# Kernel tuning notes

Measured on AMD Instinct MI355X. Metric: run time of the kernel, lower is better.

## Reference

```python
import jax, jax.numpy as jnp
import numpy as np
import math

N_WIRES = 8

def _cnot(state, ctrl, tgt):
    # state: (N, 2,2,...,2) with wire w on axis 1+w
    c_ax = 1 + ctrl
    t_ax = 1 + tgt
    s0 = jnp.take(state, 0, axis=c_ax)
    s1 = jnp.take(state, 1, axis=c_ax)
    t2 = t_ax - 1 if t_ax > c_ax else t_ax
    s1 = jnp.flip(s1, axis=t2)
    return jnp.stack([s0, s1], axis=c_ax)

def _qlayer(x, phi):
    # x: (N, 8) encoder RX angles; phi: (8,) trainable RX angles.
    # encoder RX(x_i) followed by RX(phi_i) on the same wire == RX(x_i + phi_i)
    N = x.shape[0]
    half = 0.5 * (x + phi)
    c = jnp.cos(half).astype(jnp.complex64)
    s = jnp.sin(half).astype(jnp.complex64)
    amp = jnp.stack([c, (-1j) * s], axis=-1)  # (N, 8, 2) per-wire RX|0>
    # product state via successive outer products -> (N, 2,...,2)
    state = amp[:, 0]
    for w in range(1, N_WIRES):
        q = amp[:, w].reshape((N,) + (1,) * w + (2,))
        state = state[..., None] * q
    # CNOT ring
    for w in range(N_WIRES - 1):
        state = _cnot(state, w, w + 1)
    state = _cnot(state, N_WIRES - 1, 0)
    probs = state.real ** 2 + state.imag ** 2  # (N, 2,...,2)
    exps = []
    for w in range(N_WIRES):
        axes = tuple(a for a in range(1, N_WIRES + 1) if a != 1 + w)
        pw = jnp.sum(probs, axis=axes)  # (N, 2)
        exps.append(pw[:, 0] - pw[:, 1])  # <Z_w>
    return jnp.stack(exps, axis=-1)  # (N, 8)


def setup_inputs() -> dict:
    key = jax.random.key(0)
    k1, k2, k3 = jax.random.split(key, 3)
    B, S, E = 4, 1024, 128
    x = jax.random.normal(k1, (B, S, E), jnp.float32)
    phi = jax.random.normal(k2, (N_WIRES,), jnp.float32)
    W = jax.random.normal(k3, (E, E), jnp.float32) / math.sqrt(E)
    b = jnp.zeros((E,), jnp.float32)
    return {"x": x, "phi": phi, "W": W, "b": b}


def reference(x, phi, W, b):
    B, S, E = x.shape
    H = 16
    d = N_WIRES  # head dim == n_wires == 8
    xh = x.reshape(B, S, H, d).reshape(-1, d)
    proj = _qlayer(xh, phi).reshape(B, S, H, d)
    # q, k, v are identical (same layer, same input, deterministic) -> compute once
    q = jnp.transpose(proj, (0, 2, 1, 3))  # (B, H, S, d)
    scores = jnp.einsum('bhqd,bhkd->bhqk', q, q) / math.sqrt(d)
    attn = jax.nn.softmax(scores, axis=-1)  # dropout: eval mode (identity)
    out = jnp.einsum('bhqk,bhkd->bhqd', attn, q)
    out = jnp.transpose(out, (0, 2, 1, 3)).reshape(B, S, E)
    return out @ W.T + b
```

## Files before the change

kernel.cpp:

```cpp
#include <hip/hip_runtime.h>

#define NB 4
#define NS 1024
#define NE 128
#define NH 16
#define ND 8

typedef __attribute__((ext_vector_type(4))) _Float16 half4v;
typedef __attribute__((ext_vector_type(8))) _Float16 half8v;
typedef __attribute__((ext_vector_type(2))) _Float16 half2v;
typedef __attribute__((ext_vector_type(4))) float float4v;

#if __has_builtin(__builtin_amdgcn_exp2f)
#define EXP2F(x) __builtin_amdgcn_exp2f(x)
#else
#define EXP2F(x) __expf(0.69314718055994531f * (x))
#endif

#define SQRT_ALPHA 0.71423656f

#define MFMA32(A, B, C) __builtin_amdgcn_mfma_f32_16x16x32_f16((A), (B), (C), 0, 0, 0)

static __device__ __forceinline__ half8v cat8(half4v lo, half4v hi) {
    return __builtin_shufflevector(lo, hi, 0, 1, 2, 3, 4, 5, 6, 7);
}
static __device__ __forceinline__ half4v cat4(half2v lo, half2v hi) {
    return __builtin_shufflevector(lo, hi, 0, 1, 2, 3);
}

__global__ __launch_bounds__(512, 4)
void qattn_kernel(const float* __restrict__ x, const float* __restrict__ phi,
                  float* __restrict__ aout)
{
    __shared__ __align__(16) _Float16 Klds[NS][8];
    __shared__ __align__(16) _Float16 Vt[9][1036];
    __shared__ __align__(16) float4 scratch[2][2][4][64];

    const int t    = threadIdx.x;
    const int blk  = blockIdx.x;
    const int qt   = blk & 7;
    const int bh   = blk >> 3;
    const int b    = bh >> 4;
    const int h    = bh & 15;
    const int lane = t & 63;
    const int w    = t >> 6;
    const int qg   = w & 1;
    const int kh   = w >> 1;

    const float ph0 = phi[0], ph1 = phi[1], ph2 = phi[2], ph3 = phi[3];
    const float ph4 = phi[4], ph5 = phi[5], ph6 = phi[6], ph7 = phi[7];

    {
        const float* xb = x + ((size_t)b * NS) * NE + h * ND;
        const int k0 = t, k1 = t + 512;
        float4 xa0 = *(const float4*)(xb + (size_t)k0 * NE);
        float4 xc0 = *(const float4*)(xb + (size_t)k0 * NE + 4);
        float4 xa1 = *(const float4*)(xb + (size_t)k1 * NE);
        float4 xc1 = *(const float4*)(xb + (size_t)k1 * NE + 4);
#pragma unroll
        for (int half = 0; half < 2; ++half) {
            const int k = half ? k1 : k0;
            const float4 xa = half ? xa1 : xa0;
            const float4 xc = half ? xc1 : xc0;
            float g0 = __cosf(xa.x + ph0), g1 = __cosf(xa.y + ph1);
            float g2 = __cosf(xa.z + ph2), g3 = __cosf(xa.w + ph3);
            float g4 = __cosf(xc.x + ph4), g5 = __cosf(xc.y + ph5);
            float g6 = __cosf(xc.z + ph6), g7 = __cosf(xc.w + ph7);
            float s7 = g7, s6 = s7 * g6, s5 = s6 * g5, s4 = s5 * g4, s3 = s4 * g3, s2 = s3 * g2;
            float v0 = s2 * g1;
            float v1 = g0 * g1, v2 = v1 * g2, v3 = v2 * g3;
            float v4 = v3 * g4, v5 = v4 * g5, v6 = v5 * g6, v7 = v6 * g7;
            half8v row;
            row[0] = (_Float16)(SQRT_ALPHA * v0); row[1] = (_Float16)(SQRT_ALPHA * v1);
            row[2] = (_Float16)(SQRT_ALPHA * v2); row[3] = (_Float16)(SQRT_ALPHA * v3);
            row[4] = (_Float16)(SQRT_ALPHA * v4); row[5] = (_Float16)(SQRT_ALPHA * v5);
            row[6] = (_Float16)(SQRT_ALPHA * v6); row[7] = (_Float16)(SQRT_ALPHA * v7);
            *(half8v*)&Klds[k][0] = row;
            Vt[0][k] = (_Float16)v0; Vt[1][k] = (_Float16)v1;
            Vt[2][k] = (_Float16)v2; Vt[3][k] = (_Float16)v3;
            Vt[4][k] = (_Float16)v4; Vt[5][k] = (_Float16)v5;
            Vt[6][k] = (_Float16)v6; Vt[7][k] = (_Float16)v7;
            Vt[8][k] = (_Float16)1.0f;
        }
    }
    __syncthreads();

    const int e = lane & 15;
    const int g = lane >> 4;
    const half4v zero4 = (half4v)(_Float16)0.0f;

    half4v qf0 = zero4, qf1 = zero4, qf2 = zero4, qf3 = zero4;
    if (lane < 32) {
        const int qbase = qt * 128 + qg * 64 + e;
        qf0 = *(const half4v*)&Klds[qbase][g * 4];
        qf1 = *(const half4v*)&Klds[qbase + 16][g * 4];
        qf2 = *(const half4v*)&Klds[qbase + 32][g * 4];
        qf3 = *(const half4v*)&Klds[qbase + 48][g * 4];
    }
    const half8v qf80 = cat8(qf0, zero4);
    const half8v qf81 = cat8(qf1, zero4);
    const half8v qf82 = cat8(qf2, zero4);
    const half8v qf83 = cat8(qf3, zero4);

    const _Float16* kp = &Klds[kh * 256 + e][(g & 1) * 4];
    const int ecl = (e > 8) ? 8 : e;
    const _Float16* vp = &Vt[ecl][kh * 256 + g * 4];

    float4v acc0 = (float4v)0.0f;
    float4v acc1 = (float4v)0.0f;
    float4v acc2 = (float4v)0.0f;
    float4v acc3 = (float4v)0.0f;
    const float4v zero = (float4v)0.0f;

#pragma unroll 1
    for (int p = 0; p < 8; ++p) {
        const _Float16* kpp = kp + p * 256;
        const _Float16* vpp = vp + p * 32;

        half4v kf0 = *(const half4v*)(kpp);
        half4v kf1 = *(const half4v*)(kpp + 128);
        half4v vf0 = *(const half4v*)(vpp);
        half4v vf1 = *(const half4v*)(vpp + 16);
        half8v kf80 = cat8(kf0, zero4);
        half8v kf81 = cat8(kf1, zero4);
        half8v vf8  = cat8(vf0, vf1);

        __builtin_amdgcn_s_setprio(1);
        float4v s00 = MFMA32(kf80, qf80, zero);
        float4v s01 = MFMA32(kf80, qf81, zero);
        float4v s02 = MFMA32(kf80, qf82, zero);
        float4v s03 = MFMA32(kf80, qf83, zero);
        float p000 = EXP2F(s00[0]), p001 = EXP2F(s00[1]), p002 = EXP2F(s00[2]), p003 = EXP2F(s00[3]);
        float p010 = EXP2F(s01[0]), p011 = EXP2F(s01[1]), p012 = EXP2F(s01[2]), p013 = EXP2F(s01[3]);
        float p020 = EXP2F(s02[0]), p021 = EXP2F(s02[1]), p022 = EXP2F(s02[2]), p023 = EXP2F(s02[3]);
        float p030 = EXP2F(s03[0]), p031 = EXP2F(s03[1]), p032 = EXP2F(s03[2]), p033 = EXP2F(s03[3]);
        half4v paA0 = cat4(__builtin_bit_cast(half2v, __builtin_amdgcn_cvt_pkrtz(p000, p001)),
                           __builtin_bit_cast(half2v, __builtin_amdgcn_cvt_pkrtz(p002, p003)));
        half4v paA1 = cat4(__builtin_bit_cast(half2v, __builtin_amdgcn_cvt_pkrtz(p010, p011)),
                           __builtin_bit_cast(half2v, __builtin_amdgcn_cvt_pkrtz(p012, p013)));
        half4v paA2 = cat4(__builtin_bit_cast(half2v, __builtin_amdgcn_cvt_pkrtz(p020, p021)),
                           __builtin_bit_cast(half2v, __builtin_amdgcn_cvt_pkrtz(p022, p023)));
        half4v paA3 = cat4(__builtin_bit_cast(half2v, __builtin_amdgcn_cvt_pkrtz(p030, p031)),
                           __builtin_bit_cast(half2v, __builtin_amdgcn_cvt_pkrtz(p032, p033)));
        float4v s10 = MFMA32(kf81, qf80, zero);
        float4v s11 = MFMA32(kf81, qf81, zero);
        float4v s12 = MFMA32(kf81, qf82, zero);
        float4v s13 = MFMA32(kf81, qf83, zero);
        float p100 = EXP2F(s10[0]), p101 = EXP2F(s10[1]), p102 = EXP2F(s10[2]), p103 = EXP2F(s10[3]);
        float p110 = EXP2F(s11[0]), p111 = EXP2F(s11[1]), p112 = EXP2F(s11[2]), p113 = EXP2F(s11[3]);
        float p120 = EXP2F(s12[0]), p121 = EXP2F(s12[1]), p122 = EXP2F(s12[2]), p123 = EXP2F(s12[3]);
        float p130 = EXP2F(s13[0]), p131 = EXP2F(s13[1]), p132 = EXP2F(s13[2]), p133 = EXP2F(s13[3]);
        half4v paB0 = cat4(__builtin_bit_cast(half2v, __builtin_amdgcn_cvt_pkrtz(p100, p101)),
                           __builtin_bit_cast(half2v, __builtin_amdgcn_cvt_pkrtz(p102, p103)));
        half4v paB1 = cat4(__builtin_bit_cast(half2v, __builtin_amdgcn_cvt_pkrtz(p110, p111)),
                           __builtin_bit_cast(half2v, __builtin_amdgcn_cvt_pkrtz(p112, p113)));
        half4v paB2 = cat4(__builtin_bit_cast(half2v, __builtin_amdgcn_cvt_pkrtz(p120, p121)),
                           __builtin_bit_cast(half2v, __builtin_amdgcn_cvt_pkrtz(p122, p123)));
        half4v paB3 = cat4(__builtin_bit_cast(half2v, __builtin_amdgcn_cvt_pkrtz(p130, p131)),
                           __builtin_bit_cast(half2v, __builtin_amdgcn_cvt_pkrtz(p132, p133)));

        acc0 = MFMA32(cat8(paA0, paB0), vf8, acc0);
        acc1 = MFMA32(cat8(paA1, paB1), vf8, acc1);
        acc2 = MFMA32(cat8(paA2, paB2), vf8, acc2);
        acc3 = MFMA32(cat8(paA3, paB3), vf8, acc3);
        __builtin_amdgcn_s_setprio(0);
    }

    if (kh >= 2) {
        scratch[kh - 2][qg][0][lane] = make_float4(acc0[0], acc0[1], acc0[2], acc0[3]);
        scratch[kh - 2][qg][1][lane] = make_float4(acc1[0], acc1[1], acc1[2], acc1[3]);
        scratch[kh - 2][qg][2][lane] = make_float4(acc2[0], acc2[1], acc2[2], acc2[3]);
        scratch[kh - 2][qg][3][lane] = make_float4(acc3[0], acc3[1], acc3[2], acc3[3]);
    }
    __syncthreads();
    if (kh < 2) {
        float4 c0 = scratch[kh][qg][0][lane];
        float4 c1 = scratch[kh][qg][1][lane];
        float4 c2 = scratch[kh][qg][2][lane];
        float4 c3 = scratch[kh][qg][3][lane];
        acc0[0] += c0.x; acc0[1] += c0.y; acc0[2] += c0.z; acc0[3] += c0.w;
        acc1[0] += c1.x; acc1[1] += c1.y; acc1[2] += c1.z; acc1[3] += c1.w;
        acc2[0] += c2.x; acc2[1] += c2.y; acc2[2] += c2.z; acc2[3] += c2.w;
        acc3[0] += c3.x; acc3[1] += c3.y; acc3[2] += c3.z; acc3[3] += c3.w;
    }
    if (kh == 1) {
        scratch[1][qg][0][lane] = make_float4(acc0[0], acc0[1], acc0[2], acc0[3]);
        scratch[1][qg][1][lane] = make_float4(acc1[0], acc1[1], acc1[2], acc1[3]);
        scratch[1][qg][2][lane] = make_float4(acc2[0], acc2[1], acc2[2], acc2[3]);
        scratch[1][qg][3][lane] = make_float4(acc3[0], acc3[1], acc3[2], acc3[3]);
    }
    __syncthreads();
    if (kh == 0) {
        float4 c0 = scratch[1][qg][0][lane];
        float4 c1 = scratch[1][qg][1][lane];
        float4 c2 = scratch[1][qg][2][lane];
        float4 c3 = scratch[1][qg][3][lane];
        acc0[0] += c0.x; acc0[1] += c0.y; acc0[2] += c0.z; acc0[3] += c0.w;
        acc1[0] += c1.x; acc1[1] += c1.y; acc1[2] += c1.z; acc1[3] += c1.w;
        acc2[0] += c2.x; acc2[1] += c2.y; acc2[2] += c2.z; acc2[3] += c2.w;
        acc3[0] += c3.x; acc3[1] += c3.y; acc3[2] += c3.z; acc3[3] += c3.w;

        const int src = (lane & 48) | 8;
        const size_t rb = (size_t)(b * NS + qt * 128 + qg * 64 + g * 4);
        float* opb = aout + rb * NE + h * ND + e;
#pragma unroll
        for (int qs = 0; qs < 4; ++qs) {
            float4v a = (qs == 0) ? acc0 : (qs == 1) ? acc1 : (qs == 2) ? acc2 : acc3;
            float d0 = __shfl(a[0], src, 64);
            float d1 = __shfl(a[1], src, 64);
            float d2 = __shfl(a[2], src, 64);
            float d3 = __shfl(a[3], src, 64);
            if (e < 8) {
                float* op = opb + (size_t)(qs * 16) * NE;
                op[0 * NE] = a[0] / d0;
                op[1 * NE] = a[1] / d1;
                op[2 * NE] = a[2] / d2;
                op[3 * NE] = a[3] / d3;
            }
        }
    }
}

__global__ __launch_bounds__(256)
void proj_kernel(const float* __restrict__ A, const float* __restrict__ W,
                 const float* __restrict__ bias, float* __restrict__ out)
{
    __shared__ __align__(16) _Float16 Wh[NE][140];
    __shared__ __align__(16) _Float16 As[16][140];

    const int t  = threadIdx.x;
    const int r0 = blockIdx.x * 16;

    for (int i = t; i < 16 * 32; i += 256) {
        int m = i >> 5, k4 = (i & 31) * 4;
        float4 a4 = *(const float4*)&A[(size_t)(r0 + m) * NE + k4];
        half2v h01 = __builtin_bit_cast(half2v, __builtin_amdgcn_cvt_pkrtz(a4.x, a4.y));
        half2v h23 = __builtin_bit_cast(half2v, __builtin_amdgcn_cvt_pkrtz(a4.z, a4.w));
        *(half4v*)&As[m][k4] = __builtin_shufflevector(h01, h23, 0, 1, 2, 3);
    }
    for (int i = t; i < NE * 32; i += 256) {
        int n = i >> 5, k4 = (i & 31) * 4;
        float4 w4 = *(const float4*)&W[(size_t)n * NE + k4];
        half2v h01 = __builtin_bit_cast(half2v, __builtin_amdgcn_cvt_pkrtz(w4.x, w4.y));
        half2v h23 = __builtin_bit_cast(half2v, __builtin_amdgcn_cvt_pkrtz(w4.z, w4.w));
        *(half4v*)&Wh[n][k4] = __builtin_shufflevector(h01, h23, 0, 1, 2, 3);
    }
    __syncthreads();

    const int lane = t & 63;
    const int wv   = t >> 6;
    const int e    = lane & 15;
    const int g    = lane >> 4;

    float4v acc0 = (float4v)0.0f;
    float4v acc1 = (float4v)0.0f;

#pragma unroll
    for (int c = 0; c < 8; ++c) {
        half4v af  = *(const half4v*)&As[e][c * 16 + g * 4];
        half4v bf0 = *(const half4v*)&Wh[wv * 32 + e][c * 16 + g * 4];
        half4v bf1 = *(const half4v*)&Wh[wv * 32 + 16 + e][c * 16 + g * 4];
        acc0 = __builtin_amdgcn_mfma_f32_16x16x16f16(af, bf0, acc0, 0, 0, 0);
        acc1 = __builtin_amdgcn_mfma_f32_16x16x16f16(af, bf1, acc1, 0, 0, 0);
    }

    const float bv0 = bias[wv * 32 + e];
    const float bv1 = bias[wv * 32 + 16 + e];
    float* ob = out + (size_t)(r0 + g * 4) * NE + wv * 32 + e;
#pragma unroll
    for (int r = 0; r < 4; ++r) {
        ob[(size_t)r * NE]      = acc0[r] + bv0;
        ob[(size_t)r * NE + 16] = acc1[r] + bv1;
    }
}

extern "C" void kernel_launch(void* const* d_in, const int* in_sizes, int n_in,
                              void* d_out, int out_size, void* d_ws, size_t ws_size,
                              hipStream_t stream)
{
    (void)in_sizes; (void)n_in; (void)out_size; (void)d_ws; (void)ws_size;
    const float* x   = (const float*)d_in[0];
    const float* phi = (const float*)d_in[1];
    const float* W   = (const float*)d_in[2];
    const float* b   = (const float*)d_in[3];
    float* out = (float*)d_out;

    qattn_kernel<<<dim3(NB * NH * 8), dim3(512), 0, stream>>>(x, phi, out);
    proj_kernel<<<dim3(NB * NS / 16), dim3(256), 0, stream>>>(out, W, b, out);
}
```

Baseline: 21.93 us.

## Double attention block to 1024 threads and use 16x16x16 MFMA for scores

The attention block grows from 512 to 1024 threads, so each wave handles 32 query rows instead of 64, with four query groups per key quarter. The QK score MFMAs switch from zero-padded 16x16x32 to native 16x16x16, which removes the wasted half of each score instruction. The K tile gets a 12-half row stride in LDS, likely to reduce bank conflicts, and the setprio hints are dropped. More waves per block add latency hiding at the cost of more per-wave V fragment loads and a larger reduction scratch.

```diff
diff --git a/kernel.cpp b/kernel.cpp
--- a/kernel.cpp
+++ b/kernel.cpp
@@ -19,6 +19,7 @@
 
 #define SQRT_ALPHA 0.71423656f
 
+#define MFMA16(A, B, C) __builtin_amdgcn_mfma_f32_16x16x16f16((A), (B), (C), 0, 0, 0)
 #define MFMA32(A, B, C) __builtin_amdgcn_mfma_f32_16x16x32_f16((A), (B), (C), 0, 0, 0)
 
 static __device__ __forceinline__ half8v cat8(half4v lo, half4v hi) {
@@ -28,13 +29,13 @@
     return __builtin_shufflevector(lo, hi, 0, 1, 2, 3);
 }
 
-__global__ __launch_bounds__(512, 4)
+__global__ __launch_bounds__(1024, 8)
 void qattn_kernel(const float* __restrict__ x, const float* __restrict__ phi,
                   float* __restrict__ aout)
 {
-    __shared__ __align__(16) _Float16 Klds[NS][8];
+    __shared__ __align__(16) _Float16 KA[NS * 12];
     __shared__ __align__(16) _Float16 Vt[9][1036];
-    __shared__ __align__(16) float4 scratch[2][2][4][64];
+    __shared__ __align__(16) float4 scratch[2][4][2][64];
 
     const int t    = threadIdx.x;
     const int blk  = blockIdx.x;
@@ -44,168 +45,118 @@
     const int h    = bh & 15;
     const int lane = t & 63;
     const int w    = t >> 6;
-    const int qg   = w & 1;
-    const int kh   = w >> 1;
-
-    const float ph0 = phi[0], ph1 = phi[1], ph2 = phi[2], ph3 = phi[3];
-    const float ph4 = phi[4], ph5 = phi[5], ph6 = phi[6], ph7 = phi[7];
+    const int qg   = w & 3;
+    const int kh   = w >> 2;
 
     {
-        const float* xb = x + ((size_t)b * NS) * NE + h * ND;
-        const int k0 = t, k1 = t + 512;
-        float4 xa0 = *(const float4*)(xb + (size_t)k0 * NE);
-        float4 xc0 = *(const float4*)(xb + (size_t)k0 * NE + 4);
-        float4 xa1 = *(const float4*)(xb + (size_t)k1 * NE);
-        float4 xc1 = *(const float4*)(xb + (size_t)k1 * NE + 4);
-#pragma unroll
-        for (int half = 0; half < 2; ++half) {
-            const int k = half ? k1 : k0;
-            const float4 xa = half ? xa1 : xa0;
-            const float4 xc = half ? xc1 : xc0;
-            float g0 = __cosf(xa.x + ph0), g1 = __cosf(xa.y + ph1);
-            float g2 = __cosf(xa.z + ph2), g3 = __cosf(xa.w + ph3);
-            float g4 = __cosf(xc.x + ph4), g5 = __cosf(xc.y + ph5);
-            float g6 = __cosf(xc.z + ph6), g7 = __cosf(xc.w + ph7);
-            float s7 = g7, s6 = s7 * g6, s5 = s6 * g5, s4 = s5 * g4, s3 = s4 * g3, s2 = s3 * g2;
-            float v0 = s2 * g1;
-            float v1 = g0 * g1, v2 = v1 * g2, v3 = v2 * g3;
-            float v4 = v3 * g4, v5 = v4 * g5, v6 = v5 * g6, v7 = v6 * g7;
-            half8v row;
-            row[0] = (_Float16)(SQRT_ALPHA * v0); row[1] = (_Float16)(SQRT_ALPHA * v1);
-            row[2] = (_Float16)(SQRT_ALPHA * v2); row[3] = (_Float16)(SQRT_ALPHA * v3);
-            row[4] = (_Float16)(SQRT_ALPHA * v4); row[5] = (_Float16)(SQRT_ALPHA * v5);
-            row[6] = (_Float16)(SQRT_ALPHA * v6); row[7] = (_Float16)(SQRT_ALPHA * v7);
-            *(half8v*)&Klds[k][0] = row;
-            Vt[0][k] = (_Float16)v0; Vt[1][k] = (_Float16)v1;
-            Vt[2][k] = (_Float16)v2; Vt[3][k] = (_Float16)v3;
-            Vt[4][k] = (_Float16)v4; Vt[5][k] = (_Float16)v5;
-            Vt[6][k] = (_Float16)v6; Vt[7][k] = (_Float16)v7;
-            Vt[8][k] = (_Float16)1.0f;
-        }
+        const int k = t;
+        const float* xr = x + ((size_t)(b * NS + k)) * NE + h * ND;
+        float4 xa = *(const float4*)xr;
+        float4 xc = *(const float4*)(xr + 4);
+        float g0 = __cosf(xa.x + phi[0]), g1 = __cosf(xa.y + phi[1]);
+        float g2 = __cosf(xa.z + phi[2]), g3 = __cosf(xa.w + phi[3]);
+        float g4 = __cosf(xc.x + phi[4]), g5 = __cosf(xc.y + phi[5]);
+        float g6 = __cosf(xc.z + phi[6]), g7 = __cosf(xc.w + phi[7]);
+        float s7 = g7, s6 = s7 * g6, s5 = s6 * g5, s4 = s5 * g4, s3 = s4 * g3, s2 = s3 * g2;
+        float v0 = s2 * g1;
+        float v1 = g0 * g1, v2 = v1 * g2, v3 = v2 * g3;
+        float v4 = v3 * g4, v5 = v4 * g5, v6 = v5 * g6, v7 = v6 * g7;
+        half4v rlo, rhi;
+        rlo[0] = (_Float16)(SQRT_ALPHA * v0); rlo[1] = (_Float16)(SQRT_ALPHA * v1);
+        rlo[2] = (_Float16)(SQRT_ALPHA * v2); rlo[3] = (_Float16)(SQRT_ALPHA * v3);
+        rhi[0] = (_Float16)(SQRT_ALPHA * v4); rhi[1] = (_Float16)(SQRT_ALPHA * v5);
+        rhi[2] = (_Float16)(SQRT_ALPHA * v6); rhi[3] = (_Float16)(SQRT_ALPHA * v7);
+        *(half4v*)&KA[k * 12]     = rlo;
+        *(half4v*)&KA[k * 12 + 4] = rhi;
+        Vt[0][k] = (_Float16)v0; Vt[1][k] = (_Float16)v1;
+        Vt[2][k] = (_Float16)v2; Vt[3][k] = (_Float16)v3;
+        Vt[4][k] = (_Float16)v4; Vt[5][k] = (_Float16)v5;
+        Vt[6][k] = (_Float16)v6; Vt[7][k] = (_Float16)v7;
+        Vt[8][k] = (_Float16)1.0f;
     }
     __syncthreads();
 
     const int e = lane & 15;
     const int g = lane >> 4;
-    const half4v zero4 = (half4v)(_Float16)0.0f;
-
-    half4v qf0 = zero4, qf1 = zero4, qf2 = zero4, qf3 = zero4;
+
+    half4v qf0 = (half4v)(_Float16)0.0f;
+    half4v qf1 = (half4v)(_Float16)0.0f;
     if (lane < 32) {
-        const int qbase = qt * 128 + qg * 64 + e;
-        qf0 = *(const half4v*)&Klds[qbase][g * 4];
-        qf1 = *(const half4v*)&Klds[qbase + 16][g * 4];
-        qf2 = *(const half4v*)&Klds[qbase + 32][g * 4];
-        qf3 = *(const half4v*)&Klds[qbase + 48][g * 4];
-    }
-    const half8v qf80 = cat8(qf0, zero4);
-    const half8v qf81 = cat8(qf1, zero4);
-    const half8v qf82 = cat8(qf2, zero4);
-    const half8v qf83 = cat8(qf3, zero4);
-
-    const _Float16* kp = &Klds[kh * 256 + e][(g & 1) * 4];
+        const int qrow = qt * 128 + qg * 32 + e;
+        qf0 = *(const half4v*)&KA[qrow * 12 + g * 4];
+        qf1 = *(const half4v*)&KA[(qrow + 16) * 12 + g * 4];
+    }
+
+    const _Float16* kp = &KA[(kh * 256 + e) * 12 + (g & 1) * 4];
     const int ecl = (e > 8) ? 8 : e;
     const _Float16* vp = &Vt[ecl][kh * 256 + g * 4];
 
     float4v acc0 = (float4v)0.0f;
     float4v acc1 = (float4v)0.0f;
-    float4v acc2 = (float4v)0.0f;
-    float4v acc3 = (float4v)0.0f;
     const float4v zero = (float4v)0.0f;
 
 #pragma unroll 1
     for (int p = 0; p < 8; ++p) {
-        const _Float16* kpp = kp + p * 256;
+        const _Float16* kpp = kp + p * 384;
         const _Float16* vpp = vp + p * 32;
 
         half4v kf0 = *(const half4v*)(kpp);
-        half4v kf1 = *(const half4v*)(kpp + 128);
+        half4v kf1 = *(const half4v*)(kpp + 192);
         half4v vf0 = *(const half4v*)(vpp);
         half4v vf1 = *(const half4v*)(vpp + 16);
-        half8v kf80 = cat8(kf0, zero4);
-        half8v kf81 = cat8(kf1, zero4);
-        half8v vf8  = cat8(vf0, vf1);
-
-        __builtin_amdgcn_s_setprio(1);
-        float4v s00 = MFMA32(kf80, qf80, zero);
-        float4v s01 = MFMA32(kf80, qf81, zero);
-        float4v s02 = MFMA32(kf80, qf82, zero);
-        float4v s03 = MFMA32(kf80, qf83, zero);
+
+        float4v s00 = MFMA16(kf0, qf0, zero);
+        float4v s01 = MFMA16(kf0, qf1, zero);
+        float4v s10 = MFMA16(kf1, qf0, zero);
+        float4v s11 = MFMA16(kf1, qf1, zero);
+
         float p000 = EXP2F(s00[0]), p001 = EXP2F(s00[1]), p002 = EXP2F(s00[2]), p003 = EXP2F(s00[3]);
         float p010 = EXP2F(s01[0]), p011 = EXP2F(s01[1]), p012 = EXP2F(s01[2]), p013 = EXP2F(s01[3]);
-        float p020 = EXP2F(s02[0]), p021 = EXP2F(s02[1]), p022 = EXP2F(s02[2]), p023 = EXP2F(s02[3]);
-        float p030 = EXP2F(s03[0]), p031 = EXP2F(s03[1]), p032 = EXP2F(s03[2]), p033 = EXP2F(s03[3]);
+        float p100 = EXP2F(s10[0]), p101 = EXP2F(s10[1]), p102 = EXP2F(s10[2]), p103 = EXP2F(s10[3]);
+        float p110 = EXP2F(s11[0]), p111 = EXP2F(s11[1]), p112 = EXP2F(s11[2]), p113 = EXP2F(s11[3]);
+
         half4v paA0 = cat4(__builtin_bit_cast(half2v, __builtin_amdgcn_cvt_pkrtz(p000, p001)),
                            __builtin_bit_cast(half2v, __builtin_amdgcn_cvt_pkrtz(p002, p003)));
         half4v paA1 = cat4(__builtin_bit_cast(half2v, __builtin_amdgcn_cvt_pkrtz(p010, p011)),
                            __builtin_bit_cast(half2v, __builtin_amdgcn_cvt_pkrtz(p012, p013)));
-        half4v paA2 = cat4(__builtin_bit_cast(half2v, __builtin_amdgcn_cvt_pkrtz(p020, p021)),
-                           __builtin_bit_cast(half2v, __builtin_amdgcn_cvt_pkrtz(p022, p023)));
-        half4v paA3 = cat4(__builtin_bit_cast(half2v, __builtin_amdgcn_cvt_pkrtz(p030, p031)),
-                           __builtin_bit_cast(half2v, __builtin_amdgcn_cvt_pkrtz(p032, p033)));
-        float4v s10 = MFMA32(kf81, qf80, zero);
-        float4v s11 = MFMA32(kf81, qf81, zero);
-        float4v s12 = MFMA32(kf81, qf82, zero);
-        float4v s13 = MFMA32(kf81, qf83, zero);
-        float p100 = EXP2F(s10[0]), p101 = EXP2F(s10[1]), p102 = EXP2F(s10[2]), p103 = EXP2F(s10[3]);
-        float p110 = EXP2F(s11[0]), p111 = EXP2F(s11[1]), p112 = EXP2F(s11[2]), p113 = EXP2F(s11[3]);
-        float p120 = EXP2F(s12[0]), p121 = EXP2F(s12[1]), p122 = EXP2F(s12[2]), p123 = EXP2F(s12[3]);
-        float p130 = EXP2F(s13[0]), p131 = EXP2F(s13[1]), p132 = EXP2F(s13[2]), p133 = EXP2F(s13[3]);
         half4v paB0 = cat4(__builtin_bit_cast(half2v, __builtin_amdgcn_cvt_pkrtz(p100, p101)),
                            __builtin_bit_cast(half2v, __builtin_amdgcn_cvt_pkrtz(p102, p103)));
         half4v paB1 = cat4(__builtin_bit_cast(half2v, __builtin_amdgcn_cvt_pkrtz(p110, p111)),
                            __builtin_bit_cast(half2v, __builtin_amdgcn_cvt_pkrtz(p112, p113)));
-        half4v paB2 = cat4(__builtin_bit_cast(half2v, __builtin_amdgcn_cvt_pkrtz(p120, p121)),
-                           __builtin_bit_cast(half2v, __builtin_amdgcn_cvt_pkrtz(p122, p123)));
-        half4v paB3 = cat4(__builtin_bit_cast(half2v, __builtin_amdgcn_cvt_pkrtz(p130, p131)),
-                           __builtin_bit_cast(half2v, __builtin_amdgcn_cvt_pkrtz(p132, p133)));
-
+
+        half8v vf8 = cat8(vf0, vf1);
         acc0 = MFMA32(cat8(paA0, paB0), vf8, acc0);
         acc1 = MFMA32(cat8(paA1, paB1), vf8, acc1);
-        acc2 = MFMA32(cat8(paA2, paB2), vf8, acc2);
-        acc3 = MFMA32(cat8(paA3, paB3), vf8, acc3);
-        __builtin_amdgcn_s_setprio(0);
     }
 
     if (kh >= 2) {
         scratch[kh - 2][qg][0][lane] = make_float4(acc0[0], acc0[1], acc0[2], acc0[3]);
         scratch[kh - 2][qg][1][lane] = make_float4(acc1[0], acc1[1], acc1[2], acc1[3]);
-        scratch[kh - 2][qg][2][lane] = make_float4(acc2[0], acc2[1], acc2[2], acc2[3]);
-        scratch[kh - 2][qg][3][lane] = make_float4(acc3[0], acc3[1], acc3[2], acc3[3]);
     }
     __syncthreads();
     if (kh < 2) {
         float4 c0 = scratch[kh][qg][0][lane];
         float4 c1 = scratch[kh][qg][1][lane];
-        float4 c2 = scratch[kh][qg][2][lane];
-        float4 c3 = scratch[kh][qg][3][lane];
         acc0[0] += c0.x; acc0[1] += c0.y; acc0[2] += c0.z; acc0[3] += c0.w;
         acc1[0] += c1.x; acc1[1] += c1.y; acc1[2] += c1.z; acc1[3] += c1.w;
-        acc2[0] += c2.x; acc2[1] += c2.y; acc2[2] += c2.z; acc2[3] += c2.w;
-        acc3[0] += c3.x; acc3[1] += c3.y; acc3[2] += c3.z; acc3[3] += c3.w;
     }
     if (kh == 1) {
         scratch[1][qg][0][lane] = make_float4(acc0[0], acc0[1], acc0[2], acc0[3]);
         scratch[1][qg][1][lane] = make_float4(acc1[0], acc1[1], acc1[2], acc1[3]);
-        scratch[1][qg][2][lane] = make_float4(acc2[0], acc2[1], acc2[2], acc2[3]);
-        scratch[1][qg][3][lane] = make_float4(acc3[0], acc3[1], acc3[2], acc3[3]);
     }
     __syncthreads();
     if (kh == 0) {
         float4 c0 = scratch[1][qg][0][lane];
         float4 c1 = scratch[1][qg][1][lane];
-        float4 c2 = scratch[1][qg][2][lane];
-        float4 c3 = scratch[1][qg][3][lane];
         acc0[0] += c0.x; acc0[1] += c0.y; acc0[2] += c0.z; acc0[3] += c0.w;
         acc1[0] += c1.x; acc1[1] += c1.y; acc1[2] += c1.z; acc1[3] += c1.w;
-        acc2[0] += c2.x; acc2[1] += c2.y; acc2[2] += c2.z; acc2[3] += c2.w;
-        acc3[0] += c3.x; acc3[1] += c3.y; acc3[2] += c3.z; acc3[3] += c3.w;
 
         const int src = (lane & 48) | 8;
-        const size_t rb = (size_t)(b * NS + qt * 128 + qg * 64 + g * 4);
+        const size_t rb = (size_t)(b * NS + qt * 128 + qg * 32 + g * 4);
         float* opb = aout + rb * NE + h * ND + e;
 #pragma unroll
-        for (int qs = 0; qs < 4; ++qs) {
-            float4v a = (qs == 0) ? acc0 : (qs == 1) ? acc1 : (qs == 2) ? acc2 : acc3;
+        for (int qs = 0; qs < 2; ++qs) {
+            float4v a = qs ? acc1 : acc0;
             float d0 = __shfl(a[0], src, 64);
             float d1 = __shfl(a[1], src, 64);
             float d2 = __shfl(a[2], src, 64);
@@ -285,6 +236,6 @@
     const float* b   = (const float*)d_in[3];
     float* out = (float*)d_out;
 
-    qattn_kernel<<<dim3(NB * NH * 8), dim3(512), 0, stream>>>(x, phi, out);
+    qattn_kernel<<<dim3(NB * NH * 8), dim3(1024), 0, stream>>>(x, phi, out);
     proj_kernel<<<dim3(NB * NS / 16), dim3(256), 0, stream>>>(out, W, b, out);
 }
```

After: 20.88 us. 4.8% less time.
